# Kernel tuning notes

Measured on AMD Instinct MI355X. Metric: run time of the kernel, lower is better.

## Reference

```python
import jax, jax.numpy as jnp
import numpy as np

B, D, L = 16, 64, 2048
NUM_TOKENS = 8192


def setup_inputs() -> dict:
    key = jax.random.key(0)
    k1, k2 = jax.random.split(key)
    z_e = jax.random.normal(k1, (B, D, L), dtype=jnp.float32)
    codebook = jax.random.normal(k2, (NUM_TOKENS, D), dtype=jnp.float32)
    return {"z_e": z_e, "codebook": codebook}


def reference(z_e, codebook):
    # z_e: [B, D, L] -> per-position vectors [B, L, D]
    x = jnp.transpose(z_e, (0, 2, 1))          # [B, L, D]
    xf = x.reshape(-1, x.shape[-1])            # [N, D], N = B*L
    x2 = jnp.sum(xf * xf, axis=-1, keepdims=True)            # [N, 1]
    c2 = jnp.sum(codebook * codebook, axis=-1)               # [K]
    d2 = x2 - 2.0 * (xf @ codebook.T) + c2[None, :]          # [N, K]
    idx = jnp.argmin(d2, axis=-1)                            # [N]
    zq = codebook[idx]                                        # [N, D] gather
    zq = zq.reshape(x.shape)                                  # [B, L, D]
    # straight-through with codebook stop-gradient (code_sg=True)
    zq_st = x + jax.lax.stop_gradient(zq - x)                 # [B, L, D]
    v_q = jnp.transpose(zq_st, (0, 2, 1))                     # [B, D, L]
    indices = idx.reshape(z_e.shape[0], -1)                   # [B, L]
    return v_q, indices
```

## Files before the change

### kernel.cpp

```cpp
#include <hip/hip_runtime.h>
#include <cstdint>

#define BB 16
#define DD 64
#define LL 2048
#define NQ (BB*LL)
#define KK 8192
#define VQ_SIZE (BB*DD*LL)
#define CHUNK 256
#define NCH (KK/CHUNK)
#define QSL 256
#define QPS (NQ/QSL)
#define MARGIN 0.75f

typedef __attribute__((ext_vector_type(8))) short short8;
typedef __attribute__((ext_vector_type(4))) float f32x4;
typedef unsigned long long u64;


static __device__ inline short f2bf(float f) {
    uint32_t u = __float_as_uint(f);
    uint32_t r = (u + 0x7FFFu + ((u >> 16) & 1u)) >> 16;
    return (short)r;
}

#define FMIN_DPP(v, ctrl)                                                     \
    do {                                                                      \
        int _vi = __float_as_int(v);                                          \
        int _sh = __builtin_amdgcn_update_dpp(_vi, _vi, (ctrl), 0xf, 0xf, false); \
        (v) = fminf((v), __int_as_float(_sh));                                \
    } while (0)

__global__ __launch_bounds__(256) void prep_x(const float* __restrict__ ze,
                                              short* __restrict__ xb) {
    __shared__ float t[64][65];
    const int b = blockIdx.x;
    const int l0 = blockIdx.y * 64;
    const int tid = threadIdx.x;
    #pragma unroll
    for (int it = 0; it < 4; ++it) {
        int id = it * 256 + tid;
        int d = id >> 4;
        int lw = (id & 15) * 4;
        const float4 v = *(const float4*)(ze + ((size_t)b * DD + d) * LL + l0 + lw);
        t[d][lw + 0] = v.x; t[d][lw + 1] = v.y; t[d][lw + 2] = v.z; t[d][lw + 3] = v.w;
    }
    __syncthreads();
    #pragma unroll
    for (int it = 0; it < 2; ++it) {
        int id = it * 256 + tid;
        int lr = id >> 3;
        int u = id & 7;
        short8 o;
        #pragma unroll
        for (int e = 0; e < 8; ++e) o[e] = f2bf(t[u * 8 + e][lr]);
        *(short8*)(xb + (size_t)(b * LL + l0 + lr) * DD + u * 8) = o;
    }
}

__global__ __launch_bounds__(256) void prep_xf(const float* __restrict__ ze,
                                               float* __restrict__ xf) {
    __shared__ float t[64][65];
    const int b = blockIdx.x;
    const int l0 = blockIdx.y * 64;
    const int tid = threadIdx.x;
    #pragma unroll
    for (int it = 0; it < 4; ++it) {
        int id = it * 256 + tid;
        int d = id >> 4;
        int lw = (id & 15) * 4;
        const float4 v = *(const float4*)(ze + ((size_t)b * DD + d) * LL + l0 + lw);
        t[d][lw + 0] = v.x; t[d][lw + 1] = v.y; t[d][lw + 2] = v.z; t[d][lw + 3] = v.w;
    }
    __syncthreads();
    #pragma unroll
    for (int it = 0; it < 4; ++it) {
        int id = it * 256 + tid;
        int row = id >> 4;
        int u = id & 15;
        float4 o = make_float4(t[4 * u + 0][row], t[4 * u + 1][row],
                               t[4 * u + 2][row], t[4 * u + 3][row]);
        *(float4*)(xf + (size_t)(b * LL + l0 + row) * DD + u * 4) = o;
    }
}

__global__ __launch_bounds__(256) void prep_nh2(const float* __restrict__ cbf,
                                                float* __restrict__ nh2) {
    int k = blockIdx.x * 256 + threadIdx.x;
    const float4* c4 = (const float4*)(cbf + (size_t)k * DD);
    float s = 0.f;
    #pragma unroll
    for (int i = 0; i < DD / 4; ++i) {
        float4 v = c4[i];
        s += v.x * v.x + v.y * v.y + v.z * v.z + v.w * v.w;
    }
    nh2[k] = -0.5f * s;
}

__global__ __launch_bounds__(256) void vq_screen(const float* __restrict__ cbf,
                                                 const float* __restrict__ nh2,
                                                 const short* __restrict__ xb,
                                                 float* __restrict__ cmaxT) {
    __shared__ short cbt[CHUNK * 64];
    __shared__ float sh2[CHUNK];
    const int tid = threadIdx.x;
    const int lane = tid & 63;
    const int wid = tid >> 6;
    const int kbase = blockIdx.y * CHUNK;
    const int qbase = blockIdx.x * 256 + wid * 64;
    const int r16 = lane & 15, g = lane >> 4;

    #pragma unroll
    for (int it = 0; it < 8; ++it) {
        int id = it * 256 + tid;
        int row = id >> 3;
        int u = id & 7;
        const float4 lo = *(const float4*)(cbf + (size_t)(kbase + row) * 64 + u * 8);
        const float4 hi = *(const float4*)(cbf + (size_t)(kbase + row) * 64 + u * 8 + 4);
        short8 o;
        o[0] = f2bf(lo.x); o[1] = f2bf(lo.y); o[2] = f2bf(lo.z); o[3] = f2bf(lo.w);
        o[4] = f2bf(hi.x); o[5] = f2bf(hi.y); o[6] = f2bf(hi.z); o[7] = f2bf(hi.w);
        *(short8*)(&cbt[row * 64 + ((u ^ (row & 7)) * 8)]) = o;
    }
    sh2[tid] = nh2[kbase + tid];
    __syncthreads();

    short8 a[4][2];
    #pragma unroll
    for (int t = 0; t < 4; ++t)
        #pragma unroll
        for (int ks = 0; ks < 2; ++ks)
            a[t][ks] = *(const short8*)(xb + (size_t)(qbase + t * 16 + r16) * 64 + ks * 32 + g * 8);

    float rm[4][4];
    #pragma unroll
    for (int t = 0; t < 4; ++t)
        #pragma unroll
        for (int j = 0; j < 4; ++j) rm[t][j] = -3.4e38f;

    for (int cs = 0; cs < CHUNK / 16; ++cs) {
        const int rowb = cs * 16 + r16;
        const float nh = sh2[rowb];
        const f32x4 ci = {nh, nh, nh, nh};
        const short8 b0 = *(const short8*)(&cbt[rowb * 64 + ((g ^ (rowb & 7)) * 8)]);
        const short8 b1 = *(const short8*)(&cbt[rowb * 64 + (((g + 4) ^ (rowb & 7)) * 8)]);
        #pragma unroll
        for (int t = 0; t < 4; ++t) {
            f32x4 acc = __builtin_amdgcn_mfma_f32_16x16x32_bf16(a[t][0], b0, ci, 0, 0, 0);
            acc = __builtin_amdgcn_mfma_f32_16x16x32_bf16(a[t][1], b1, acc, 0, 0, 0);
            rm[t][0] = fmaxf(rm[t][0], acc[0]);
            rm[t][1] = fmaxf(rm[t][1], acc[1]);
            rm[t][2] = fmaxf(rm[t][2], acc[2]);
            rm[t][3] = fmaxf(rm[t][3], acc[3]);
        }
    }

    #pragma unroll
    for (int s = 1; s < 16; s <<= 1)
        #pragma unroll
        for (int t = 0; t < 4; ++t)
            #pragma unroll
            for (int j = 0; j < 4; ++j)
                rm[t][j] = fmaxf(rm[t][j], __shfl_xor(rm[t][j], s));

    if (r16 == 0) {
        #pragma unroll
        for (int t = 0; t < 4; ++t)
            #pragma unroll
            for (int j = 0; j < 4; ++j)
                cmaxT[(size_t)blockIdx.y * NQ + (qbase + t * 16 + g * 4 + j)] = rm[t][j];
    }
}

__global__ __launch_bounds__(256) void vq_cand(const float* __restrict__ cmaxT,
                                               u64* __restrict__ qmask,
                                               u64* __restrict__ keys) {
    const int tid = threadIdx.x;
    const int lane = tid & 63;
    const int q = blockIdx.x * 256 + tid;
    const int qword = q >> 6;
    float v[NCH];
    float m = -3.4e38f;
    #pragma unroll
    for (int j = 0; j < NCH; ++j) {
        v[j] = cmaxT[(size_t)j * NQ + q];
        m = fmaxf(m, v[j]);
    }
    keys[q] = ~0ULL;
    const float thr = m - MARGIN;
    #pragma unroll
    for (int j = 0; j < NCH; ++j) {
        u64 mm = __ballot(v[j] >= thr);
        if (lane == 0) qmask[(size_t)j * (NQ / 64) + qword] = mm;
    }
}

__global__ __launch_bounds__(256) void vq_exact(const float* __restrict__ xf,
                                                const float* __restrict__ cbf,
                                                const float* __restrict__ nh2,
                                                const u64* __restrict__ qmask,
                                                u64* __restrict__ keys) {
    const int ch = blockIdx.x;
    const int slice = blockIdx.y;
    const int lane = threadIdx.x & 63;
    const int wid = threadIdx.x >> 6;
    const int kb = ch * CHUNK + wid * 64;
    const int k = kb + lane;

    const u64* wm = qmask + (size_t)ch * (NQ / 64) + slice * (QPS / 64);
    u64 words[QPS / 64];
    u64 any = 0;
    #pragma unroll
    for (int w = 0; w < QPS / 64; ++w) {
        u64 x = wm[w];
        uint32_t lo = __builtin_amdgcn_readfirstlane((uint32_t)x);
        uint32_t hi = __builtin_amdgcn_readfirstlane((uint32_t)(x >> 32));
        words[w] = ((u64)hi << 32) | lo;
        any |= words[w];
    }
    if (!any) return;

    float cdv[64];
    #pragma unroll
    for (int i = 0; i < 16; ++i)
        *(float4*)&cdv[4 * i] = *(const float4*)(cbf + (size_t)k * DD + 4 * i);
    const float nh2k = nh2[k];

    #pragma unroll 1
    for (int w = 0; w < QPS / 64; ++w) {
        u64 sw = words[w];
        while (sw) {
            const int bit = __ffsll((long long)sw) - 1;
            sw &= sw - 1;
            const int q = slice * QPS + w * 64 + bit;
            const float4* xr4 = (const float4*)(xf + (size_t)q * DD);
            float4 xv[16];
            #pragma unroll
            for (int i = 0; i < 16; ++i) xv[i] = xr4[i];

            float a0 = 0.f, a1 = 0.f, a2 = 0.f, a3 = 0.f;
            #pragma unroll
            for (int i = 0; i < 16; ++i) {
                a0 = fmaf(xv[i].x, cdv[4 * i + 0], a0);
                a1 = fmaf(xv[i].y, cdv[4 * i + 1], a1);
                a2 = fmaf(xv[i].z, cdv[4 * i + 2], a2);
                a3 = fmaf(xv[i].w, cdv[4 * i + 3], a3);
            }
            float val = -(((a0 + a1) + (a2 + a3)) + nh2k);

            float mn = val;
            FMIN_DPP(mn, 0x111);
            FMIN_DPP(mn, 0x112);
            FMIN_DPP(mn, 0x114);
            FMIN_DPP(mn, 0x118);
            FMIN_DPP(mn, 0x142);
            FMIN_DPP(mn, 0x143);
            const float mnall = __uint_as_float(
                __builtin_amdgcn_readlane(__float_as_uint(mn), 63));

            u64 mk = __ballot(val == mnall);
            int srcl = __ffsll((long long)mk) - 1;
            uint32_t uu = __float_as_uint(mnall);
            uint32_t ub = ((int)uu < 0) ? ~uu : (uu | 0x80000000u);
            u64 key = ((u64)ub << 32) | (unsigned)(kb + srcl);
            if (lane == 0) atomicMin(&keys[q], key);
        }
    }
}

__global__ __launch_bounds__(256) void vq_gather(const float* __restrict__ cb,
                                                 const u64* __restrict__ keys,
                                                 float* __restrict__ vq,
                                                 float* __restrict__ oidx) {
    int t = blockIdx.x * 256 + threadIdx.x;
    int l = t & (LL - 1);
    int bd = t >> 11;
    int d = bd & 63;
    int b = bd >> 6;
    int idx = (int)(unsigned)(keys[b * LL + l] & 0x1FFFu);
    vq[t] = cb[idx * DD + d];
    if (d == 0) oidx[b * LL + l] = (float)idx;
}

extern "C" void kernel_launch(void* const* d_in, const int* in_sizes, int n_in,
                              void* d_out, int out_size, void* d_ws, size_t ws_size,
                              hipStream_t stream) {
    const float* ze = (const float*)d_in[0];
    const float* cb = (const float*)d_in[1];
    float* out = (float*)d_out;

    short* xb = (short*)d_out;
    float* cmaxT = (float*)((char*)d_out + (size_t)NQ * DD * 2);
    float* xf = (float*)d_out;
    u64* qmask = (u64*)(out + VQ_SIZE);
    float* nh2 = (float*)d_ws;
    u64* keys = (u64*)((char*)d_ws + (size_t)KK * 4);
    float* oidx = out + VQ_SIZE;

    dim3 gx(BB, LL / 64);
    prep_x<<<gx, 256, 0, stream>>>(ze, xb);
    prep_nh2<<<KK / 256, 256, 0, stream>>>(cb, nh2);

    dim3 gs(NQ / 256, NCH);
    vq_screen<<<gs, 256, 0, stream>>>(cb, nh2, xb, cmaxT);

    vq_cand<<<NQ / 256, 256, 0, stream>>>(cmaxT, qmask, keys);

    prep_xf<<<gx, 256, 0, stream>>>(ze, xf);

    dim3 ge(NCH, QSL);
    vq_exact<<<ge, 256, 0, stream>>>(xf, cb, nh2, qmask, keys);

    vq_gather<<<VQ_SIZE / 256, 256, 0, stream>>>(cb, keys, out, oidx);
}
```

Before: 161.2 us.

## Double query tile per wave in screen kernel and use DPP row max reduction

```diff
diff --git a/kernel.cpp b/kernel.cpp
--- a/kernel.cpp
+++ b/kernel.cpp
@@ -1,4 +1,5 @@
 #include <hip/hip_runtime.h>
+#include <hip/hip_bf16.h>
 #include <cstdint>
 
 #define BB 16
@@ -19,9 +20,8 @@
 
 
 static __device__ inline short f2bf(float f) {
-    uint32_t u = __float_as_uint(f);
-    uint32_t r = (u + 0x7FFFu + ((u >> 16) & 1u)) >> 16;
-    return (short)r;
+    __hip_bfloat16 h = __float2bfloat16(f);
+    return __builtin_bit_cast(short, h);
 }
 
 #define FMIN_DPP(v, ctrl)                                                     \
@@ -29,6 +29,13 @@
         int _vi = __float_as_int(v);                                          \
         int _sh = __builtin_amdgcn_update_dpp(_vi, _vi, (ctrl), 0xf, 0xf, false); \
         (v) = fminf((v), __int_as_float(_sh));                                \
+    } while (0)
+
+#define FMAX_DPP(v, ctrl)                                                     \
+    do {                                                                      \
+        int _vi = __float_as_int(v);                                          \
+        int _sh = __builtin_amdgcn_update_dpp(_vi, _vi, (ctrl), 0xf, 0xf, false); \
+        (v) = fmaxf((v), __int_as_float(_sh));                                \
     } while (0)
 
 __global__ __launch_bounds__(256) void prep_x(const float* __restrict__ ze,
@@ -107,7 +114,7 @@
     const int lane = tid & 63;
     const int wid = tid >> 6;
     const int kbase = blockIdx.y * CHUNK;
-    const int qbase = blockIdx.x * 256 + wid * 64;
+    const int qbase = blockIdx.x * 512 + wid * 128;
     const int r16 = lane & 15, g = lane >> 4;
 
     #pragma unroll
@@ -125,16 +132,16 @@
     sh2[tid] = nh2[kbase + tid];
     __syncthreads();
 
-    short8 a[4][2];
-    #pragma unroll
-    for (int t = 0; t < 4; ++t)
+    short8 a[8][2];
+    #pragma unroll
+    for (int t = 0; t < 8; ++t)
         #pragma unroll
         for (int ks = 0; ks < 2; ++ks)
             a[t][ks] = *(const short8*)(xb + (size_t)(qbase + t * 16 + r16) * 64 + ks * 32 + g * 8);
 
-    float rm[4][4];
-    #pragma unroll
-    for (int t = 0; t < 4; ++t)
+    float rm[8][4];
+    #pragma unroll
+    for (int t = 0; t < 8; ++t)
         #pragma unroll
         for (int j = 0; j < 4; ++j) rm[t][j] = -3.4e38f;
 
@@ -145,7 +152,7 @@
         const short8 b0 = *(const short8*)(&cbt[rowb * 64 + ((g ^ (rowb & 7)) * 8)]);
         const short8 b1 = *(const short8*)(&cbt[rowb * 64 + (((g + 4) ^ (rowb & 7)) * 8)]);
         #pragma unroll
-        for (int t = 0; t < 4; ++t) {
+        for (int t = 0; t < 8; ++t) {
             f32x4 acc = __builtin_amdgcn_mfma_f32_16x16x32_bf16(a[t][0], b0, ci, 0, 0, 0);
             acc = __builtin_amdgcn_mfma_f32_16x16x32_bf16(a[t][1], b1, acc, 0, 0, 0);
             rm[t][0] = fmaxf(rm[t][0], acc[0]);
@@ -156,16 +163,18 @@
     }
 
     #pragma unroll
-    for (int s = 1; s < 16; s <<= 1)
-        #pragma unroll
-        for (int t = 0; t < 4; ++t)
-            #pragma unroll
-            for (int j = 0; j < 4; ++j)
-                rm[t][j] = fmaxf(rm[t][j], __shfl_xor(rm[t][j], s));
-
-    if (r16 == 0) {
-        #pragma unroll
-        for (int t = 0; t < 4; ++t)
+    for (int t = 0; t < 8; ++t)
+        #pragma unroll
+        for (int j = 0; j < 4; ++j) {
+            FMAX_DPP(rm[t][j], 0x111);
+            FMAX_DPP(rm[t][j], 0x112);
+            FMAX_DPP(rm[t][j], 0x114);
+            FMAX_DPP(rm[t][j], 0x118);
+        }
+
+    if (r16 == 15) {
+        #pragma unroll
+        for (int t = 0; t < 8; ++t)
             #pragma unroll
             for (int j = 0; j < 4; ++j)
                 cmaxT[(size_t)blockIdx.y * NQ + (qbase + t * 16 + g * 4 + j)] = rm[t][j];
@@ -195,11 +204,11 @@
     }
 }
 
-__global__ __launch_bounds__(256) void vq_exact(const float* __restrict__ xf,
-                                                const float* __restrict__ cbf,
-                                                const float* __restrict__ nh2,
-                                                const u64* __restrict__ qmask,
-                                                u64* __restrict__ keys) {
+__global__ __launch_bounds__(256, 2) void vq_exact(const float* __restrict__ xf,
+                                                   const float* __restrict__ cbf,
+                                                   const float* __restrict__ nh2,
+                                                   const u64* __restrict__ qmask,
+                                                   u64* __restrict__ keys) {
     const int ch = blockIdx.x;
     const int slice = blockIdx.y;
     const int lane = threadIdx.x & 63;
@@ -220,10 +229,10 @@
     }
     if (!any) return;
 
-    float cdv[64];
-    #pragma unroll
-    for (int i = 0; i < 16; ++i)
-        *(float4*)&cdv[4 * i] = *(const float4*)(cbf + (size_t)k * DD + 4 * i);
+    f32x4 cdv[16];
+    const f32x4* cb4 = (const f32x4*)(cbf + (size_t)k * DD);
+    #pragma unroll
+    for (int i = 0; i < 16; ++i) cdv[i] = cb4[i];
     const float nh2k = nh2[k];
 
     #pragma unroll 1
@@ -233,18 +242,18 @@
             const int bit = __ffsll((long long)sw) - 1;
             sw &= sw - 1;
             const int q = slice * QPS + w * 64 + bit;
-            const float4* xr4 = (const float4*)(xf + (size_t)q * DD);
-            float4 xv[16];
+            const f32x4* xr4 = (const f32x4*)(xf + (size_t)q * DD);
+            f32x4 xv[16];
             #pragma unroll
             for (int i = 0; i < 16; ++i) xv[i] = xr4[i];
 
             float a0 = 0.f, a1 = 0.f, a2 = 0.f, a3 = 0.f;
             #pragma unroll
             for (int i = 0; i < 16; ++i) {
-                a0 = fmaf(xv[i].x, cdv[4 * i + 0], a0);
-                a1 = fmaf(xv[i].y, cdv[4 * i + 1], a1);
-                a2 = fmaf(xv[i].z, cdv[4 * i + 2], a2);
-                a3 = fmaf(xv[i].w, cdv[4 * i + 3], a3);
+                a0 = fmaf(xv[i].x, cdv[i].x, a0);
+                a1 = fmaf(xv[i].y, cdv[i].y, a1);
+                a2 = fmaf(xv[i].z, cdv[i].z, a2);
+                a3 = fmaf(xv[i].w, cdv[i].w, a3);
             }
             float val = -(((a0 + a1) + (a2 + a3)) + nh2k);
 
@@ -301,7 +310,7 @@
     prep_x<<<gx, 256, 0, stream>>>(ze, xb);
     prep_nh2<<<KK / 256, 256, 0, stream>>>(cb, nh2);
 
-    dim3 gs(NQ / 256, NCH);
+    dim3 gs(NQ / 512, NCH);
     vq_screen<<<gs, 256, 0, stream>>>(cb, nh2, xb, cmaxT);
 
     vq_cand<<<NQ / 256, 256, 0, stream>>>(cmaxT, qmask, keys);
```

Result: faster. 153.8 us (-4.5%).
